# Performance work log

Measured on AMD Instinct MI355X. Metric: run time of the kernel, lower is better.

## Reference

```python
import jax, jax.numpy as jnp
import numpy as np

D_MODEL = 1024
D_HIDDEN = 2048
BATCH = 2
SEQ = 4096


def setup_inputs() -> dict:
    key = jax.random.key(0)
    ks = jax.random.split(key, 14)
    d, h = D_MODEL, D_HIDDEN
    s_d = 1.0 / np.sqrt(d)
    s_h = 1.0 / np.sqrt(h)
    x = jax.random.normal(ks[0], (BATCH, SEQ, d), jnp.float32)
    W1 = jax.random.normal(ks[1], (d, d), jnp.float32) * s_d
    W2 = jax.random.normal(ks[2], (d, d), jnp.float32) * s_d
    Wlast = jax.random.normal(ks[3], (d, d), jnp.float32) * s_d
    conv_w = jax.random.normal(ks[4], (d, 1, 3), jnp.float32) * 0.5  # depthwise (O, I/g=1, K)
    conv_b = jnp.zeros((d,), jnp.float32)
    A = jax.random.normal(ks[5], (h,), jnp.float32)
    Wb = jax.random.normal(ks[6], (h, d), jnp.float32) * s_d
    bb = jnp.zeros((h,), jnp.float32)
    Wc = jax.random.normal(ks[7], (d, h), jnp.float32) * s_h
    bc = jnp.zeros((d,), jnp.float32)
    Wd = jax.random.normal(ks[8], (d, d), jnp.float32) * s_d
    bd = jnp.zeros((d,), jnp.float32)
    # small delta so cumsum(delta*A) over SEQ steps stays O(1) (avoids exp overflow)
    Wdelta = jax.random.normal(ks[9], (h, d), jnp.float32) * 0.01
    bdelta = jnp.full((h,), -8.0, jnp.float32)
    return dict(x=x, W1=W1, conv_w=conv_w, conv_b=conv_b, A=A, Wb=Wb, bb=bb,
                Wc=Wc, bc=bc, Wd=Wd, bd=bd, Wdelta=Wdelta, bdelta=bdelta,
                W2=W2, Wlast=Wlast)


def reference(x, W1, conv_w, conv_b, A, Wb, bb, Wc, bc, Wd, bd, Wdelta, bdelta, W2, Wlast):
    # x: [B, L, d]
    x1 = x @ W1.T  # linear1 (no bias)
    # depthwise conv1d, kernel 3, pad 1, groups = d_model
    xc = jax.lax.conv_general_dilated(
        x1.transpose(0, 2, 1), conv_w,
        window_strides=(1,), padding=[(1, 1)],
        feature_group_count=D_MODEL,
        dimension_numbers=('NCH', 'OIH', 'NCH')) + conv_b[None, :, None]
    xa = jax.nn.silu(xc.transpose(0, 2, 1))  # [B, L, d]
    # SSM: delta/A/B discretization + cumprod-cumsum scan along sequence
    delta = jax.nn.softplus(xa @ Wdelta.T + bdelta)  # [B, L, h]
    A_bar = jnp.exp(delta * A)
    B_bar = delta * (xa @ Wb.T + bb)
    A_cum = jnp.cumprod(A_bar, axis=1)
    h_st = jnp.cumsum(B_bar / A_cum, axis=1) * A_cum  # [B, L, h]
    out_ssm = (h_st @ Wc.T + bc) + (xa @ Wd.T + bd)  # [B, L, d]
    # gated residual
    x_res = jax.nn.silu(out_ssm @ W2.T)
    z = out_ssm * x_res
    return out_ssm + z @ Wlast.T
```

## Files before the change

### kernel.cpp

```cpp
#include <hip/hip_runtime.h>
#include <cstdint>
#include <cstddef>

#define DMODEL 1024
#define DH 2048
#define BATCH 2
#define SEQ 4096
#define MROWS (BATCH*SEQ)
#define CHUNK 64
#define NCHUNK (SEQ/CHUNK)

typedef unsigned short u16;
typedef __attribute__((ext_vector_type(8))) short bf16x8;
typedef __attribute__((ext_vector_type(4))) float f32x4;

__device__ __forceinline__ u16 f2bf(float f) {
    union { float f; unsigned u; } v; v.f = f;
    unsigned r = v.u + 0x7FFFu + ((v.u >> 16) & 1u);
    return (u16)(r >> 16);
}
__device__ __forceinline__ float bf2f(u16 h) {
    union { unsigned u; float f; } v; v.u = ((unsigned)h) << 16; return v.f;
}

__device__ __forceinline__ float softplus_fast(float x) {
    if (x < -4.f) return __expf(x);
    return (x > 0.f) ? (x + log1pf(__expf(-x))) : log1pf(__expf(x));
}
__device__ __forceinline__ float silu_fast(float v) {
    return v * __fdividef(1.f, 1.f + __expf(-v));
}

__global__ void cvt_bf16(const float* __restrict__ src, u16* __restrict__ dst, int n4) {
    int i = blockIdx.x * blockDim.x + threadIdx.x;
    if (i >= n4) return;
    const float4 v = reinterpret_cast<const float4*>(src)[i];
    ushort4 o;
    o.x = f2bf(v.x); o.y = f2bf(v.y); o.z = f2bf(v.z); o.w = f2bf(v.w);
    reinterpret_cast<ushort4*>(dst)[i] = o;
}

__device__ __forceinline__ void gload_lds16(const void* g, void* l) {
    __builtin_amdgcn_global_load_lds(
        (const __attribute__((address_space(1))) void*)g,
        (__attribute__((address_space(3))) void*)l,
        16, 0, 0);
}

template<int EP, bool TWOK>
__global__ __launch_bounds__(256) void gemm_bt(
    const u16* __restrict__ A1, const u16* __restrict__ B1, int K1,
    const u16* __restrict__ A2, const u16* __restrict__ B2, int K2,
    float* __restrict__ C, u16* __restrict__ Cb, u16* __restrict__ Cb2,
    const float* __restrict__ bias, const float* __restrict__ bias2,
    const float* __restrict__ aux,
    int M, int N)
{
    __shared__ u16 As[2][128*64];
    __shared__ u16 Bs[2][128*64];
    const int tid = threadIdx.x;

    const int nwg = gridDim.x * gridDim.y;
    int wg = blockIdx.y * gridDim.x + blockIdx.x;
    wg = (wg & 7) * (nwg >> 3) + (wg >> 3);
    const int m0 = (wg / gridDim.x) * 128;
    const int n0 = (wg % gridDim.x) * 128;

    const int wave = tid >> 6, lane = tid & 63;
    const int wr = (wave >> 1) * 64;
    const int wc = (wave & 1) * 64;
    const int fr = lane & 15, fq = lane >> 4;

    f32x4 acc[4][4];
    #pragma unroll
    for (int m = 0; m < 4; m++)
        #pragma unroll
        for (int n = 0; n < 4; n++) acc[m][n] = f32x4{0.f, 0.f, 0.f, 0.f};

    const int nt1 = K1 >> 6;
    const int nt  = TWOK ? nt1 + (K2 >> 6) : nt1;

    auto stage = [&](int t, int buf) {
        const u16* A = A1; const u16* B = B1; int K = K1; int k0 = t << 6;
        if (TWOK && t >= nt1) { A = A2; B = B2; K = K2; k0 = (t - nt1) << 6; }
        #pragma unroll
        for (int i = 0; i < 4; ++i) {
            const int g = i*256 + tid;
            const int r = g >> 3;
            const int ch = (g & 7) ^ (r & 7);
            gload_lds16(A + (size_t)(m0 + r)*K + (k0 + ch*8), (char*)As[buf] + (size_t)g*16);
            gload_lds16(B + (size_t)(n0 + r)*K + (k0 + ch*8), (char*)Bs[buf] + (size_t)g*16);
        }
    };

    auto compute = [&](int buf) {
        #pragma unroll
        for (int kk = 0; kk < 2; ++kk) {
            bf16x8 af[4], bfr[4];
            #pragma unroll
            for (int m = 0; m < 4; m++) {
                const int r = wr + m*16 + fr;
                af[m] = *reinterpret_cast<const bf16x8*>(
                    (const char*)As[buf] + r*128 + (((kk*4 + fq) ^ (r & 7)) * 16));
            }
            #pragma unroll
            for (int n = 0; n < 4; n++) {
                const int r = wc + n*16 + fr;
                bfr[n] = *reinterpret_cast<const bf16x8*>(
                    (const char*)Bs[buf] + r*128 + (((kk*4 + fq) ^ (r & 7)) * 16));
            }
            #pragma unroll
            for (int m = 0; m < 4; m++)
                #pragma unroll
                for (int n = 0; n < 4; n++)
                    acc[m][n] = __builtin_amdgcn_mfma_f32_16x16x32_bf16(af[m], bfr[n], acc[m][n], 0, 0, 0);
        }
    };

    stage(0, 0);
    if (nt > 1) stage(1, 1);

    int cur = 0;
    for (int t = 0; t < nt; ++t) {
        if (t < nt - 1) { asm volatile("s_waitcnt vmcnt(8)" ::: "memory"); }
        else            { asm volatile("s_waitcnt vmcnt(0)" ::: "memory"); }
        __builtin_amdgcn_s_barrier();
        __builtin_amdgcn_sched_barrier(0);
        compute(cur);
        __builtin_amdgcn_s_barrier();
        __builtin_amdgcn_sched_barrier(0);
        if (t + 2 < nt) stage(t + 2, cur);
        cur ^= 1;
    }

    #pragma unroll
    for (int m = 0; m < 4; m++) {
        #pragma unroll
        for (int n = 0; n < 4; n++) {
            const int col = n0 + wc + n*16 + fr;
            float bv = 0.f;
            if constexpr (EP != 4) {
                if (bias)  bv += bias[col];
                if (bias2) bv += bias2[col];
            }
            #pragma unroll
            for (int j = 0; j < 4; j++) {
                const int row = m0 + wr + m*16 + fq*4 + j;
                const size_t idx = (size_t)row * N + col;
                float v = acc[m][n][j] + bv;
                if constexpr (EP == 0) {
                    Cb[idx] = f2bf(v);
                } else if constexpr (EP == 1) {
                    C[idx] = v;
                    Cb[idx] = f2bf(v);
                } else if constexpr (EP == 2) {
                    Cb[idx] = f2bf(aux[idx] * silu_fast(v));
                } else if constexpr (EP == 3) {
                    C[idx] = aux[idx] + v;
                } else {
                    if (col < DH) {
                        Cb [(size_t)row*DH + col]        = f2bf(softplus_fast(v + bias[col]));
                    } else {
                        Cb2[(size_t)row*DH + (col - DH)] = f2bf(v + bias2[col - DH]);
                    }
                }
            }
        }
    }
}

__global__ void conv_silu8(const u16* __restrict__ x1, const float* __restrict__ cw,
                           const float* __restrict__ cb, u16* __restrict__ xab) {
    int t = blockIdx.x * blockDim.x + threadIdx.x;
    int c8  = t & (DMODEL/8 - 1);
    int row = t >> 7;
    int l = row & (SEQ - 1);
    const int c0 = c8 * 8;
    const size_t i0 = (size_t)row * DMODEL + c0;
    bf16x8 v0 = *reinterpret_cast<const bf16x8*>(x1 + i0);
    bf16x8 vm = {}; if (l > 0)       vm = *reinterpret_cast<const bf16x8*>(x1 + i0 - DMODEL);
    bf16x8 vp = {}; if (l < SEQ - 1) vp = *reinterpret_cast<const bf16x8*>(x1 + i0 + DMODEL);
    if (l == 0)       vm = bf16x8{};
    if (l == SEQ - 1) vp = bf16x8{};
    bf16x8 o;
    #pragma unroll
    for (int j = 0; j < 8; ++j) {
        const int c = c0 + j;
        float v = cw[c*3+0]*bf2f((u16)vm[j]) + cw[c*3+1]*bf2f((u16)v0[j])
                + cw[c*3+2]*bf2f((u16)vp[j]) + cb[c];
        o[j] = (short)f2bf(silu_fast(v));
    }
    *reinterpret_cast<bf16x8*>(xab + i0) = o;
}

__global__ void scan_chunks(const u16* __restrict__ delta, const u16* __restrict__ pBv,
                            const float* __restrict__ Avec,
                            float* __restrict__ cA, float* __restrict__ cB) {
    const int c = blockIdx.x * blockDim.x + threadIdx.x;
    const int q = blockIdx.y;
    const int b = blockIdx.z;
    const float Ac = Avec[c];
    float hA = 1.f, hB = 0.f;
    size_t base = ((size_t)b*SEQ + q*CHUNK)*DH + c;
    for (int j = 0; j < CHUNK; ++j) {
        float d = bf2f(delta[base]);
        float Abar = __expf(d * Ac);
        hA *= Abar;
        hB = Abar*hB + d * bf2f(pBv[base]);
        base += DH;
    }
    size_t o = ((size_t)b*NCHUNK + q)*DH + c;
    cA[o] = hA; cB[o] = hB;
}

__global__ void scan_prefix(const float* __restrict__ cA, const float* __restrict__ cB,
                            float* __restrict__ cH) {
    const int t = blockIdx.x * blockDim.x + threadIdx.x;
    const int b = t >> 11;
    const int c = t & (DH - 1);
    float h = 0.f;
    size_t o = ((size_t)b*NCHUNK)*DH + c;
    float a = cA[o], bb = cB[o];
    for (int q = 0; q < NCHUNK; ++q) {
        const size_t on = o + DH;
        float a2 = 0.f, b2 = 0.f;
        if (q + 1 < NCHUNK) { a2 = cA[on]; b2 = cB[on]; }
        cH[o] = h;
        h = a*h + bb;
        a = a2; bb = b2; o = on;
    }
}

__global__ void scan_apply(const u16* __restrict__ delta, const u16* __restrict__ pBv,
                           const float* __restrict__ Avec, const float* __restrict__ cH,
                           u16* __restrict__ hstb) {
    const int c = blockIdx.x * blockDim.x + threadIdx.x;
    const int q = blockIdx.y;
    const int b = blockIdx.z;
    const float Ac = Avec[c];
    float h = cH[((size_t)b*NCHUNK + q)*DH + c];
    size_t base = ((size_t)b*SEQ + q*CHUNK)*DH + c;
    for (int j = 0; j < CHUNK; ++j) {
        float d = bf2f(delta[base]);
        float Abar = __expf(d * Ac);
        h = Abar*h + d * bf2f(pBv[base]);
        hstb[base] = f2bf(h);
        base += DH;
    }
}

extern "C" void kernel_launch(void* const* d_in, const int* in_sizes, int n_in,
                              void* d_out, int out_size, void* d_ws, size_t ws_size,
                              hipStream_t stream) {
    const float* x      = (const float*)d_in[0];
    const float* W1     = (const float*)d_in[1];
    const float* conv_w = (const float*)d_in[2];
    const float* conv_b = (const float*)d_in[3];
    const float* Avec   = (const float*)d_in[4];
    const float* Wb     = (const float*)d_in[5];
    const float* bb     = (const float*)d_in[6];
    const float* Wc     = (const float*)d_in[7];
    const float* bc     = (const float*)d_in[8];
    const float* Wd     = (const float*)d_in[9];
    const float* bd     = (const float*)d_in[10];
    const float* Wdelta = (const float*)d_in[11];
    const float* bdelta = (const float*)d_in[12];
    const float* W2     = (const float*)d_in[13];
    const float* Wlast  = (const float*)d_in[14];
    float* out = (float*)d_out;
    (void)in_sizes; (void)n_in; (void)out_size;

    struct Ptrs {
        u16 *sW;
        float *cA, *cB, *cH;
        u16 *xb, *x1b, *xab, *delta, *pBv, *ossb, *hstb, *zb;
        float *oss;
        size_t total;
    };
    auto layout = [&](int passes) -> Ptrs {
        Ptrs P{};
        const size_t Mp = MROWS / passes;
        const int nb = BATCH / passes;
        size_t off = 0;
        auto al = [&](size_t bytes) -> char* {
            char* p = (char*)d_ws + off; off += (bytes + 255) & ~(size_t)255; return p;
        };
        P.sW  = (u16*)al((size_t)2*DH*DMODEL*2);
        P.cA  = (float*)al((size_t)nb*NCHUNK*DH*4);
        P.cB  = (float*)al((size_t)nb*NCHUNK*DH*4);
        P.cH  = (float*)al((size_t)nb*NCHUNK*DH*4);
        char* RA = al(Mp*DMODEL*2);
        char* RB = al(Mp*DMODEL*2);
        char* RC = al(Mp*DMODEL*2);
        char* RD = al(Mp*DH*2);
        char* RE = al(Mp*DH*2);
        char* RF = al(Mp*DH*2);
        P.xb    = (u16*)RA; P.ossb = (u16*)RA;
        P.x1b   = (u16*)RB; P.zb   = (u16*)RB;
        P.xab   = (u16*)RC;
        P.delta = (u16*)RD; P.oss  = (float*)RD;
        P.pBv   = (u16*)RE;
        P.hstb  = (u16*)RF;
        P.total = off;
        return P;
    };

    int passes = (ws_size >= layout(1).total) ? 1 : 2;
    Ptrs P = layout(passes);
    if (ws_size < P.total) return;
    const int Mp = MROWS / passes;
    const int nb = BATCH / passes;

    const dim3 blk(256);
    auto cvt = [&](const float* s, u16* d, size_t n) {
        int n4 = (int)(n / 4);
        cvt_bf16<<<dim3((n4 + 255)/256), blk, 0, stream>>>(s, d, n4);
    };
    const dim3 gD (DMODEL/128, Mp/128);
    const dim3 gDB(2*DH/128,   Mp/128);
    u16* sW2 = P.sW + (size_t)DH*DMODEL;

    for (int p = 0; p < passes; ++p) {
        const float* x_p  = x  + (size_t)p*Mp*DMODEL;
        float*      out_p = out + (size_t)p*Mp*DMODEL;

        cvt(x_p, P.xb, (size_t)Mp*DMODEL);
        cvt(W1, P.sW, (size_t)DMODEL*DMODEL);
        gemm_bt<0,false><<<gD, blk, 0, stream>>>(P.xb, P.sW, DMODEL, nullptr, nullptr, 0,
                                                 nullptr, P.x1b, nullptr, nullptr, nullptr, nullptr, Mp, DMODEL);
        conv_silu8<<<dim3(Mp*DMODEL/8/256), blk, 0, stream>>>(P.x1b, conv_w, conv_b, P.xab);
        cvt(Wdelta, P.sW, (size_t)DH*DMODEL);
        cvt(Wb,     sW2,  (size_t)DH*DMODEL);
        gemm_bt<4,false><<<gDB, blk, 0, stream>>>(P.xab, P.sW, DMODEL, nullptr, nullptr, 0,
                                                  nullptr, P.delta, P.pBv, bdelta, bb, nullptr, Mp, 2*DH);
        scan_chunks<<<dim3(DH/256, NCHUNK, nb), blk, 0, stream>>>(P.delta, P.pBv, Avec, P.cA, P.cB);
        scan_prefix<<<dim3(nb*DH/256), blk, 0, stream>>>(P.cA, P.cB, P.cH);
        scan_apply <<<dim3(DH/256, NCHUNK, nb), blk, 0, stream>>>(P.delta, P.pBv, Avec, P.cH, P.hstb);
        cvt(Wd, P.sW, (size_t)DMODEL*DMODEL);
        cvt(Wc, sW2,  (size_t)DMODEL*DH);
        gemm_bt<1,true><<<gD, blk, 0, stream>>>(P.xab, P.sW, DMODEL, P.hstb, sW2, DH,
                                                P.oss, P.ossb, nullptr, bd, bc, nullptr, Mp, DMODEL);
        cvt(W2, P.sW, (size_t)DMODEL*DMODEL);
        gemm_bt<2,false><<<gD, blk, 0, stream>>>(P.ossb, P.sW, DMODEL, nullptr, nullptr, 0,
                                                 nullptr, P.zb, nullptr, nullptr, nullptr, P.oss, Mp, DMODEL);
        cvt(Wlast, P.sW, (size_t)DMODEL*DMODEL);
        gemm_bt<3,false><<<gD, blk, 0, stream>>>(P.zb, P.sW, DMODEL, nullptr, nullptr, 0,
                                                 out_p, nullptr, nullptr, nullptr, nullptr, P.oss, Mp, DMODEL);
    }
}
```

Measured before the change: 356.2 us.

## Restructure GEMM into 8-wave 128x256 tiles with triple-buffered interleaved staging

Replaces the 4-wave 128x128 GEMM with an 8-wave kernel computing 128x256 output tiles, so each workgroup reuses its A tile across twice as many columns. LDS moves from double to triple buffering, and global-to-LDS loads for tile t+2 are split into three parts interleaved with the per-row-fragment MFMA groups. s_setprio is raised around the MFMA groups. The aim is more data reuse per workgroup and better overlap of loads with math, at the cost of more LDS per workgroup (144 KB across the three stages), which may limit occupancy, and half as many workgroups.

```diff
diff --git a/kernel.cpp b/kernel.cpp
--- a/kernel.cpp
+++ b/kernel.cpp
@@ -48,7 +48,7 @@
 }
 
 template<int EP, bool TWOK>
-__global__ __launch_bounds__(256) void gemm_bt(
+__global__ __launch_bounds__(512) void gemm8p(
     const u16* __restrict__ A1, const u16* __restrict__ B1, int K1,
     const u16* __restrict__ A2, const u16* __restrict__ B2, int K2,
     float* __restrict__ C, u16* __restrict__ Cb, u16* __restrict__ Cb2,
@@ -56,19 +56,19 @@
     const float* __restrict__ aux,
     int M, int N)
 {
-    __shared__ u16 As[2][128*64];
-    __shared__ u16 Bs[2][128*64];
+    __shared__ u16 As[3][128*64];
+    __shared__ u16 Bs[3][256*64];
     const int tid = threadIdx.x;
 
     const int nwg = gridDim.x * gridDim.y;
     int wg = blockIdx.y * gridDim.x + blockIdx.x;
     wg = (wg & 7) * (nwg >> 3) + (wg >> 3);
     const int m0 = (wg / gridDim.x) * 128;
-    const int n0 = (wg % gridDim.x) * 128;
+    const int n0 = (wg % gridDim.x) * 256;
 
     const int wave = tid >> 6, lane = tid & 63;
-    const int wr = (wave >> 1) * 64;
-    const int wc = (wave & 1) * 64;
+    const int wr = (wave >> 2) * 64;
+    const int wc = (wave & 3) * 64;
     const int fr = lane & 15, fq = lane >> 4;
 
     f32x4 acc[4][4];
@@ -80,57 +80,74 @@
     const int nt1 = K1 >> 6;
     const int nt  = TWOK ? nt1 + (K2 >> 6) : nt1;
 
-    auto stage = [&](int t, int buf) {
-        const u16* A = A1; const u16* B = B1; int K = K1; int k0 = t << 6;
-        if (TWOK && t >= nt1) { A = A2; B = B2; K = K2; k0 = (t - nt1) << 6; }
+    auto stage_part = [&](int tt, int part) {
+        const u16* A = A1; const u16* B = B1; int K = K1; int k0 = tt << 6;
+        if (TWOK && tt >= nt1) { A = A2; B = B2; K = K2; k0 = (tt - nt1) << 6; }
+        const int s = tt - (tt/3)*3;
         #pragma unroll
-        for (int i = 0; i < 4; ++i) {
-            const int g = i*256 + tid;
-            const int r = g >> 3;
-            const int ch = (g & 7) ^ (r & 7);
-            gload_lds16(A + (size_t)(m0 + r)*K + (k0 + ch*8), (char*)As[buf] + (size_t)g*16);
-            gload_lds16(B + (size_t)(n0 + r)*K + (k0 + ch*8), (char*)Bs[buf] + (size_t)g*16);
+        for (int j = 0; j < 2; ++j) {
+            const int g = j*512 + tid;
+            if (part == 0) {
+                const int r = g >> 3, ch = g & 7;
+                gload_lds16(A + (size_t)(m0 + r)*K + (k0 + ((ch ^ (r & 7)) << 3)),
+                            (char*)As[s] + (size_t)g*16);
+            } else {
+                const int r = (part-1)*128 + (g >> 3), ch = g & 7;
+                gload_lds16(B + (size_t)(n0 + r)*K + (k0 + ((ch ^ (r & 7)) << 3)),
+                            (char*)Bs[s] + (size_t)(part-1)*16384 + (size_t)g*16);
+            }
         }
     };
 
-    auto compute = [&](int buf) {
+    #pragma unroll
+    for (int part = 0; part < 3; ++part) stage_part(0, part);
+    #pragma unroll
+    for (int part = 0; part < 3; ++part) stage_part(1, part);
+    asm volatile("s_waitcnt vmcnt(6)" ::: "memory");
+    __builtin_amdgcn_s_barrier();
+    __builtin_amdgcn_sched_barrier(0);
+
+    for (int t = 0; t < nt; ++t) {
+        const int s = t - (t/3)*3;
+        const char* Ab = (const char*)As[s];
+        const char* Bb = (const char*)Bs[s];
+        bf16x8 bf[4][2];
         #pragma unroll
-        for (int kk = 0; kk < 2; ++kk) {
-            bf16x8 af[4], bfr[4];
+        for (int q = 0; q < 4; ++q) {
+            bf16x8 af[2];
+            const int ar = wr + q*16 + fr;
             #pragma unroll
-            for (int m = 0; m < 4; m++) {
-                const int r = wr + m*16 + fr;
-                af[m] = *reinterpret_cast<const bf16x8*>(
-                    (const char*)As[buf] + r*128 + (((kk*4 + fq) ^ (r & 7)) * 16));
-            }
+            for (int kk = 0; kk < 2; ++kk)
+                af[kk] = *reinterpret_cast<const bf16x8*>(
+                    Ab + ar*128 + (((kk*4 + fq) ^ (ar & 7)) * 16));
+            if (q == 0) {
+                #pragma unroll
+                for (int nf = 0; nf < 4; ++nf) {
+                    const int br = wc + nf*16 + fr;
+                    #pragma unroll
+                    for (int kk = 0; kk < 2; ++kk)
+                        bf[nf][kk] = *reinterpret_cast<const bf16x8*>(
+                            Bb + br*128 + (((kk*4 + fq) ^ (br & 7)) * 16));
+                }
+            }
+            if (q < 3 && t + 2 < nt) stage_part(t + 2, q);
+            __builtin_amdgcn_s_barrier();
+            asm volatile("s_waitcnt lgkmcnt(0)" ::: "memory");
+            __builtin_amdgcn_sched_barrier(0);
+            __builtin_amdgcn_s_setprio(1);
             #pragma unroll
-            for (int n = 0; n < 4; n++) {
-                const int r = wc + n*16 + fr;
-                bfr[n] = *reinterpret_cast<const bf16x8*>(
-                    (const char*)Bs[buf] + r*128 + (((kk*4 + fq) ^ (r & 7)) * 16));
-            }
-            #pragma unroll
-            for (int m = 0; m < 4; m++)
+            for (int nf = 0; nf < 4; ++nf)
                 #pragma unroll
-                for (int n = 0; n < 4; n++)
-                    acc[m][n] = __builtin_amdgcn_mfma_f32_16x16x32_bf16(af[m], bfr[n], acc[m][n], 0, 0, 0);
+                for (int kk = 0; kk < 2; ++kk)
+                    acc[q][nf] = __builtin_amdgcn_mfma_f32_16x16x32_bf16(af[kk], bf[nf][kk], acc[q][nf], 0, 0, 0);
+            __builtin_amdgcn_s_setprio(0);
+            if (q == 3) {
+                if (t < nt - 2) { asm volatile("s_waitcnt vmcnt(6)" ::: "memory"); }
+                else            { asm volatile("s_waitcnt vmcnt(0)" ::: "memory"); }
+            }
+            __builtin_amdgcn_s_barrier();
+            __builtin_amdgcn_sched_barrier(0);
         }
-    };
-
-    stage(0, 0);
-    if (nt > 1) stage(1, 1);
-
-    int cur = 0;
-    for (int t = 0; t < nt; ++t) {
-        if (t < nt - 1) { asm volatile("s_waitcnt vmcnt(8)" ::: "memory"); }
-        else            { asm volatile("s_waitcnt vmcnt(0)" ::: "memory"); }
-        __builtin_amdgcn_s_barrier();
-        __builtin_amdgcn_sched_barrier(0);
-        compute(cur);
-        __builtin_amdgcn_s_barrier();
-        __builtin_amdgcn_sched_barrier(0);
-        if (t + 2 < nt) stage(t + 2, cur);
-        cur ^= 1;
     }
 
     #pragma unroll
@@ -312,12 +329,13 @@
     const int nb = BATCH / passes;
 
     const dim3 blk(256);
+    const dim3 blkG(512);
     auto cvt = [&](const float* s, u16* d, size_t n) {
         int n4 = (int)(n / 4);
         cvt_bf16<<<dim3((n4 + 255)/256), blk, 0, stream>>>(s, d, n4);
     };
-    const dim3 gD (DMODEL/128, Mp/128);
-    const dim3 gDB(2*DH/128,   Mp/128);
+    const dim3 gD (DMODEL/256, Mp/128);
+    const dim3 gDB(2*DH/256,   Mp/128);
     u16* sW2 = P.sW + (size_t)DH*DMODEL;
 
     for (int p = 0; p < passes; ++p) {
@@ -326,25 +344,25 @@
 
         cvt(x_p, P.xb, (size_t)Mp*DMODEL);
         cvt(W1, P.sW, (size_t)DMODEL*DMODEL);
-        gemm_bt<0,false><<<gD, blk, 0, stream>>>(P.xb, P.sW, DMODEL, nullptr, nullptr, 0,
+        gemm8p<0,false><<<gD, blkG, 0, stream>>>(P.xb, P.sW, DMODEL, nullptr, nullptr, 0,
                                                  nullptr, P.x1b, nullptr, nullptr, nullptr, nullptr, Mp, DMODEL);
         conv_silu8<<<dim3(Mp*DMODEL/8/256), blk, 0, stream>>>(P.x1b, conv_w, conv_b, P.xab);
         cvt(Wdelta, P.sW, (size_t)DH*DMODEL);
         cvt(Wb,     sW2,  (size_t)DH*DMODEL);
-        gemm_bt<4,false><<<gDB, blk, 0, stream>>>(P.xab, P.sW, DMODEL, nullptr, nullptr, 0,
+        gemm8p<4,false><<<gDB, blkG, 0, stream>>>(P.xab, P.sW, DMODEL, nullptr, nullptr, 0,
                                                   nullptr, P.delta, P.pBv, bdelta, bb, nullptr, Mp, 2*DH);
         scan_chunks<<<dim3(DH/256, NCHUNK, nb), blk, 0, stream>>>(P.delta, P.pBv, Avec, P.cA, P.cB);
         scan_prefix<<<dim3(nb*DH/256), blk, 0, stream>>>(P.cA, P.cB, P.cH);
         scan_apply <<<dim3(DH/256, NCHUNK, nb), blk, 0, stream>>>(P.delta, P.pBv, Avec, P.cH, P.hstb);
         cvt(Wd, P.sW, (size_t)DMODEL*DMODEL);
         cvt(Wc, sW2,  (size_t)DMODEL*DH);
-        gemm_bt<1,true><<<gD, blk, 0, stream>>>(P.xab, P.sW, DMODEL, P.hstb, sW2, DH,
+        gemm8p<1,true><<<gD, blkG, 0, stream>>>(P.xab, P.sW, DMODEL, P.hstb, sW2, DH,
                                                 P.oss, P.ossb, nullptr, bd, bc, nullptr, Mp, DMODEL);
         cvt(W2, P.sW, (size_t)DMODEL*DMODEL);
-        gemm_bt<2,false><<<gD, blk, 0, stream>>>(P.ossb, P.sW, DMODEL, nullptr, nullptr, 0,
+        gemm8p<2,false><<<gD, blkG, 0, stream>>>(P.ossb, P.sW, DMODEL, nullptr, nullptr, 0,
                                                  nullptr, P.zb, nullptr, nullptr, nullptr, P.oss, Mp, DMODEL);
         cvt(Wlast, P.sW, (size_t)DMODEL*DMODEL);
-        gemm_bt<3,false><<<gD, blk, 0, stream>>>(P.zb, P.sW, DMODEL, nullptr, nullptr, 0,
+        gemm8p<3,false><<<gD, blkG, 0, stream>>>(P.zb, P.sW, DMODEL, nullptr, nullptr, 0,
                                                  out_p, nullptr, nullptr, nullptr, nullptr, P.oss, Mp, DMODEL);
     }
 }
```

Result: slower. 393.2 us (+10.4%).
